# Optimization experiments

Measured on AMD Instinct MI355X. Metric: run time of the kernel, lower is better.

The kernel has to match this reference:

```python
import math
import jax, jax.numpy as jnp
import numpy as np

B, T, DIN, D, L, H = 512, 16, 7, 512, 2, 8
FF = 4 * D
HD = D // H
NEG = -1e30


def setup_inputs() -> dict:
    key = jax.random.key(0)
    ks = jax.random.split(key, 18)
    s = 0.02
    n = lambda k, sh: jax.random.normal(k, sh, dtype=jnp.float32) * s
    return {
        "x_scalar_norm": jax.random.normal(ks[0], (B, T, DIN), dtype=jnp.float32),
        "ip_w": n(ks[1], (DIN, D)),   # input_proj (x @ W)
        "ip_b": n(ks[2], (D,)),
        "qkv_w": n(ks[3], (L, D, 3 * D)),  # packed in_proj per layer
        "qkv_b": n(ks[4], (L, 3 * D)),
        "out_w": n(ks[5], (L, D, D)),
        "out_b": n(ks[6], (L, D)),
        "ln1_s": jnp.ones((L, D), jnp.float32),
        "ln1_b": jnp.zeros((L, D), jnp.float32),
        "ff_w1": n(ks[7], (L, D, FF)),
        "ff_b1": n(ks[8], (L, FF)),
        "ff_w2": n(ks[9], (L, FF, D)),
        "ff_b2": n(ks[10], (L, D)),
        "ln2_s": jnp.ones((L, D), jnp.float32),
        "ln2_b": jnp.zeros((L, D), jnp.float32),
        "head_w": n(ks[11], (D, 3)),  # moment_head
        "head_b": n(ks[12], (3,)),
    }


def _pos_encoding(t, d):
    pos = jnp.arange(t, dtype=jnp.float32)[:, None]
    div = jnp.exp(jnp.arange(0, d, 2, dtype=jnp.float32) * (-math.log(10000.0) / d))
    pe = jnp.zeros((t, d), jnp.float32)
    pe = pe.at[:, 0::2].set(jnp.sin(pos * div))
    pe = pe.at[:, 1::2].set(jnp.cos(pos * div))
    return pe


def _ln(x, s, b, eps=1e-5):
    m = jnp.mean(x, axis=-1, keepdims=True)
    v = jnp.mean(jnp.square(x - m), axis=-1, keepdims=True)
    return (x - m) * jax.lax.rsqrt(v + eps) * s + b


def _encoder_layer(h, qkv_w, qkv_b, out_w, out_b, ln1_s, ln1_b,
                   w1, b1, w2, b2, ln2_s, ln2_b, causal):
    b, t, _ = h.shape
    qkv = h @ qkv_w + qkv_b  # [b, t, 3D]
    q, k, v = jnp.split(qkv, 3, axis=-1)
    q = q.reshape(b, t, H, HD).transpose(0, 2, 1, 3)  # bhqd
    k = k.reshape(b, t, H, HD).transpose(0, 2, 1, 3)
    v = v.reshape(b, t, H, HD).transpose(0, 2, 1, 3)
    scores = jnp.einsum('bhqd,bhkd->bhqk', q, k) / math.sqrt(HD)
    scores = jnp.where(causal[None, None], scores, NEG)
    attn = jax.nn.softmax(scores, axis=-1)
    o = jnp.einsum('bhqk,bhkd->bhqd', attn, v)
    o = o.transpose(0, 2, 1, 3).reshape(b, t, D) @ out_w + out_b
    h = _ln(h + o, ln1_s, ln1_b)           # post-norm (norm_first=False)
    ff = jax.nn.relu(h @ w1 + b1) @ w2 + b2
    return _ln(h + ff, ln2_s, ln2_b)


def reference(x_scalar_norm, ip_w, ip_b, qkv_w, qkv_b, out_w, out_b,
              ln1_s, ln1_b, ff_w1, ff_b1, ff_w2, ff_b2, ln2_s, ln2_b,
              head_w, head_b):
    b, t_total, _ = x_scalar_norm.shape
    pe = _pos_encoding(t_total, D)
    x_roll = x_scalar_norm
    preds = []
    for t in range(t_total):
        xp = x_roll[:, :t + 1, :]                 # full backbone recompute per step
        h = xp @ ip_w + ip_b + pe[None, :t + 1]
        causal = jnp.tril(jnp.ones((t + 1, t + 1), dtype=bool))
        for l in range(L):
            h = _encoder_layer(h, qkv_w[l], qkv_b[l], out_w[l], out_b[l],
                               ln1_s[l], ln1_b[l], ff_w1[l], ff_b1[l],
                               ff_w2[l], ff_b2[l], ln2_s[l], ln2_b[l], causal)
        y_t = h[:, -1, :] @ head_w + head_b       # [b, 3]
        preds.append(y_t)
        if t < t_total - 1:
            # eval mode: no teacher forcing; feed back detached prediction
            x_roll = x_roll.at[:, t + 1, DIN - 3:].set(jax.lax.stop_gradient(y_t))
    return jnp.stack(preds, axis=1)  # [b, T, 3]
```

## Files before the change

### kernel.cpp

```cpp
#include <hip/hip_runtime.h>
#include <hip/hip_bf16.h>
#include <math.h>


typedef __attribute__((__ext_vector_type__(8))) short short8;
typedef __attribute__((__ext_vector_type__(4))) float floatx4;

__device__ inline short8 as_short8(uint4 v){ union U{uint4 u; short8 s;} x; x.u=v; return x.s; }

__device__ inline ushort f2bf(float f){
    __hip_bfloat16 h = __float2bfloat16(f);
    ushort u; __builtin_memcpy(&u, &h, 2); return u;
}

__device__ inline uint32_t sld32(const void* p){
    return __hip_atomic_load((const uint32_t*)p, __ATOMIC_RELAXED, __HIP_MEMORY_SCOPE_SYSTEM);
}
__device__ inline void sst32(void* p, uint32_t v){
    __hip_atomic_store((uint32_t*)p, v, __ATOMIC_RELAXED, __HIP_MEMORY_SCOPE_SYSTEM);
}
__device__ inline unsigned long long sld64(const void* p){
    return __hip_atomic_load((const unsigned long long*)p, __ATOMIC_RELAXED, __HIP_MEMORY_SCOPE_SYSTEM);
}
__device__ inline float u2f(uint32_t u){ float f; __builtin_memcpy(&f, &u, 4); return f; }

#define WS_TMPA0 12582912
#define WS_TMPA1 13631488
#define WS_TMPB0 14680064
#define WS_TMPB1 15728640
#define WS_BAR   16777216
#define WS_KC    16779264
#define WS_VC    33556480

__global__ __launch_bounds__(256)
void swz_k(const float* __restrict__ qkv_w, const float* __restrict__ out_w,
           const float* __restrict__ ff1_w, const float* __restrict__ ff2_w,
           ushort* __restrict__ wsw)
{
    if (blockIdx.z == 0){
        float* tz = (float*)((char*)wsw + WS_TMPA0);
        int id = (blockIdx.y*gridDim.x + blockIdx.x)*256 + threadIdx.x;
        sst32(&tz[id], 0u);
        sst32(&tz[id + 524288], 0u);
        if (blockIdx.x == 0 && blockIdx.y == 0){
            unsigned* bar = (unsigned*)((char*)wsw + WS_BAR);
            for (int i = threadIdx.x; i < 512; i += 256)
                sst32(&bar[i], 0u);
        }
    }
    int id = blockIdx.z; int l = id & 1; int mi = id >> 1;
    int K, N; const float* src; size_t doff;
    if (mi == 0)      { K = 512;  N = 1536; src = qkv_w + (size_t)l*786432;  doff = (size_t)l*786432; }
    else if (mi == 1) { K = 512;  N = 512;  src = out_w + (size_t)l*262144;  doff = 1572864 + (size_t)l*262144; }
    else if (mi == 2) { K = 512;  N = 2048; src = ff1_w + (size_t)l*1048576; doff = 2097152 + (size_t)l*1048576; }
    else              { K = 2048; N = 512;  src = ff2_w + (size_t)l*1048576; doff = 4194304 + (size_t)l*1048576; }
    int n0 = blockIdx.x * 64, k0 = blockIdx.y * 32;
    if (n0 >= N || k0 >= K) return;
    __shared__ float tt[32][64];
    int tid = threadIdx.x;
    int c = tid & 63, r = tid >> 6;
    #pragma unroll
    for (int i = 0; i < 8; ++i)
        tt[r + i*4][c] = src[(size_t)(k0 + r + i*4)*N + n0 + c];
    __syncthreads();
    int q = tid >> 6, n = tid & 63;
    union { ushort s[8]; uint4 v; } pk;
    #pragma unroll
    for (int i = 0; i < 8; ++i) pk.s[i] = f2bf(tt[q*8 + i][n]);
    ((uint4*)(wsw + doff))[(size_t)((k0 >> 5)*4 + q)*N + n0 + n] = pk.v;
}

#define AOX(c, m) ((((c) << 4)) + (((m) ^ ((c) & 15))))

__global__ __launch_bounds__(1024, 1)
void mega_k(const float* __restrict__ x, const float* __restrict__ ip_w,
            const float* __restrict__ ip_b, const float* __restrict__ qkv_b,
            const float* __restrict__ out_b, const float* __restrict__ ln1_s,
            const float* __restrict__ ln1_b, const float* __restrict__ ff_b1,
            const float* __restrict__ ff_b2, const float* __restrict__ ln2_s,
            const float* __restrict__ ln2_b, const float* __restrict__ hw,
            const float* __restrict__ hb, float* __restrict__ out,
            char* __restrict__ ws)
{
    const ushort* wsw = (const ushort*)ws;
    unsigned* bar = (unsigned*)(ws + WS_BAR);
    __hip_bfloat16* kc0 = (__hip_bfloat16*)(ws + WS_KC);
    __hip_bfloat16* vc0 = (__hip_bfloat16*)(ws + WS_VC);

    const int g  = blockIdx.x & 31;
    const int j  = blockIdx.x >> 5;
    const int b0 = g * 16;
    const int tid  = threadIdx.x;
    const int lane = tid & 63, w = tid >> 6;
    const int qd = lane >> 4, ln = lane & 15;
    unsigned* cnt = bar + g*16;
    unsigned epoch = 0;

    __shared__ uint4 aLds[64*16];
    __shared__ uint4 aoLds[8*16];
    __shared__ uint4 ffLds[32*16];
    __shared__ float hL[16][516];
    __shared__ float qLds[16][68];
    __shared__ float yLds[16][3];

    auto gbar = [&]() {
        __syncthreads();
        epoch += 8;
        if (tid == 0){
            __hip_atomic_fetch_add(cnt, 1u, __ATOMIC_RELAXED, __HIP_MEMORY_SCOPE_SYSTEM);
            while (__hip_atomic_load(cnt, __ATOMIC_RELAXED, __HIP_MEMORY_SCOPE_SYSTEM) < epoch)
                __builtin_amdgcn_s_sleep(8);
        }
        __syncthreads();
    };

    for (int s = 0; s < 32; ++s){
        const int t = s >> 1, l = s & 1, p = s & 1;
        __hip_bfloat16* kc = kc0 + (size_t)l*4194304;
        __hip_bfloat16* vc = vc0 + (size_t)l*4194304;
        float* tmpA = (float*)(ws + WS_TMPA0 + (size_t)p*1048576);

        if (s == 0){
            int m = tid >> 6, cg = tid & 63;
            int b = b0 + m;
            const float* xr = x + ((size_t)b*16 + 0)*7;
            float hv[8]; union { ushort sx[8]; uint4 v; } pk;
            #pragma unroll
            for (int k = 0; k < 8; ++k){
                int d = cg*8 + k;
                float pe = (d & 1) ? 1.0f : 0.0f;
                float acc = ip_b[d] + pe
                    + xr[0]*ip_w[d]        + xr[1]*ip_w[512 + d]
                    + xr[2]*ip_w[1024 + d] + xr[3]*ip_w[1536 + d]
                    + xr[4]*ip_w[2048 + d] + xr[5]*ip_w[2560 + d] + xr[6]*ip_w[3072 + d];
                hv[k] = acc; pk.sx[k] = f2bf(acc);
                hL[m][d] = acc;
            }
            aLds[AOX(cg, m)] = pk.v;
        } else {
            const float* tB = (const float*)(ws + WS_TMPB0 + (size_t)((s-1)&1)*1048576);
            const int lp = (s-1) & 1;
            int m = w, b = b0 + m;
            const float* rowp = tB + (size_t)b*512 + lane*8;
            union { unsigned long long q[4]; float f[8]; } uu;
            uu.q[0] = sld64(rowp);     uu.q[1] = sld64(rowp + 2);
            uu.q[2] = sld64(rowp + 4); uu.q[3] = sld64(rowp + 6);
            float sm = 0.f, sq = 0.f;
            #pragma unroll
            for (int k = 0; k < 8; ++k){ sm += uu.f[k]; sq += uu.f[k]*uu.f[k]; }
            #pragma unroll
            for (int off = 32; off; off >>= 1){ sm += __shfl_xor(sm, off); sq += __shfl_xor(sq, off); }
            float mean = sm * (1.0f/512.0f);
            float var  = sq * (1.0f/512.0f) - mean*mean;
            float rs   = rsqrtf(var + 1e-5f);
            float hn[8];
            #pragma unroll
            for (int k = 0; k < 8; ++k){
                int d = lane*8 + k;
                hn[k] = (uu.f[k] - mean)*rs*ln2_s[lp*512 + d] + ln2_b[lp*512 + d];
            }
            if (l == 1){
                union { ushort sx[8]; uint4 v; } pk;
                #pragma unroll
                for (int k = 0; k < 8; ++k){ hL[m][lane*8 + k] = hn[k]; pk.sx[k] = f2bf(hn[k]); }
                aLds[AOX(lane, m)] = pk.v;
            } else {
                float sr[3] = {};
                #pragma unroll
                for (int k = 0; k < 8; ++k){
                    int d = lane*8 + k;
                    sr[0] += hn[k]*hw[d*3+0]; sr[1] += hn[k]*hw[d*3+1]; sr[2] += hn[k]*hw[d*3+2];
                }
                #pragma unroll
                for (int off = 32; off; off >>= 1){
                    sr[0] += __shfl_xor(sr[0], off);
                    sr[1] += __shfl_xor(sr[1], off);
                    sr[2] += __shfl_xor(sr[2], off);
                }
                if (lane == 0){
                    #pragma unroll
                    for (int c = 0; c < 3; ++c){
                        float y = sr[c] + hb[c];
                        yLds[m][c] = y;
                        if (j == 0) out[((size_t)b*16 + (t-1))*3 + c] = y;
                    }
                }
                __syncthreads();
                int m2 = tid >> 6, cg = tid & 63;
                int b2 = b0 + m2;
                const float* xr = x + ((size_t)b2*16 + t)*7;
                float f4 = yLds[m2][0], f5 = yLds[m2][1], f6 = yLds[m2][2];
                float hv[8]; union { ushort sx[8]; uint4 v; } pk;
                #pragma unroll
                for (int k = 0; k < 8; ++k){
                    int d = cg*8 + k;
                    int e2 = d & ~1;
                    float div = expf(-(float)e2 * (9.210340371976184f / 512.0f));
                    float arg = (float)t * div;
                    float pe = (d & 1) ? cosf(arg) : sinf(arg);
                    float acc = ip_b[d] + pe
                        + xr[0]*ip_w[d]        + xr[1]*ip_w[512 + d]
                        + xr[2]*ip_w[1024 + d] + xr[3]*ip_w[1536 + d]
                        + f4*ip_w[2048 + d]    + f5*ip_w[2560 + d] + f6*ip_w[3072 + d];
                    hv[k] = acc; pk.sx[k] = f2bf(acc);
                    hL[m2][d] = acc;
                }
                aLds[AOX(cg, m2)] = pk.v;
            }
        }
        __syncthreads();

        {
            if (w < 12){
                const uint4* Bg = (const uint4*)(wsw + (size_t)l*786432);
                int s0 = w >> 2, cs = w & 3;
                floatx4 acc = {};
                for (int kb = 0; kb < 16; ++kb){
                    short8 af = as_short8(aLds[AOX(kb*4 + qd, ln)]);
                    int n = s0*512 + j*64 + cs*16 + ln;
                    short8 bf = as_short8(Bg[(size_t)(kb*4 + qd)*1536 + n]);
                    acc = __builtin_amdgcn_mfma_f32_16x16x32_bf16(af, bf, acc, 0, 0, 0);
                }
                #pragma unroll
                for (int r = 0; r < 4; ++r){
                    int row = qd*4 + r;
                    int cc = cs*16 + ln;
                    int n = s0*512 + j*64 + cc;
                    float v = acc[r] + qkv_b[l*1536 + n];
                    int b = b0 + row;
                    if (s0 == 0) qLds[row][cc] = v;
                    else if (s0 == 1) kc[(((size_t)b*8 + j)*16 + t)*64 + cc] = __float2bfloat16(v);
                    else              vc[(((size_t)b*8 + j)*16 + t)*64 + cc] = __float2bfloat16(v);
                }
            }
        }
        __syncthreads();

        {
            int m = w, b = b0 + m;
            float q = qLds[m][lane];
            const __hip_bfloat16* kp = kc + ((size_t)b*8 + j)*1024;
            const __hip_bfloat16* vp = vc + ((size_t)b*8 + j)*1024;
            float mr = -1e30f, sden = 0.0f, o = 0.0f;
            for (int jj = 0; jj <= t; ++jj){
                float pdot = q * __bfloat162float(kp[jj*64 + lane]);
                #pragma unroll
                for (int off = 32; off; off >>= 1) pdot += __shfl_xor(pdot, off);
                pdot *= 0.125f;
                float nm = fmaxf(mr, pdot);
                float sc = __expf(mr - nm);
                float e  = __expf(pdot - nm);
                sden = sden*sc + e;
                o = o*sc + e*__bfloat162float(vp[jj*64 + lane]);
                mr = nm;
            }
            float ov = o / sden;
            ((ushort*)aoLds)[AOX(lane >> 3, m)*8 + (lane & 7)] = f2bf(ov);
        }
        __syncthreads();

        {
            const uint4* Bg = (const uint4*)(wsw + 1572864 + (size_t)l*262144);
            #pragma unroll
            for (int c2 = 0; c2 < 2; ++c2){
                int n = (w*2 + c2)*16 + ln;
                floatx4 acc = {};
                #pragma unroll
                for (int kbl = 0; kbl < 2; ++kbl){
                    short8 af = as_short8(aoLds[AOX(kbl*4 + qd, ln)]);
                    short8 bf = as_short8(Bg[(size_t)((2*j + kbl)*4 + qd)*512 + n]);
                    acc = __builtin_amdgcn_mfma_f32_16x16x32_bf16(af, bf, acc, 0, 0, 0);
                }
                #pragma unroll
                for (int r = 0; r < 4; ++r){
                    int row = qd*4 + r, b = b0 + row;
                    float v = acc[r];
                    if (j == 0) v += out_b[l*512 + n] + hL[row][n];
                    unsafeAtomicAdd(&tmpA[(size_t)b*512 + n], v);
                }
            }
        }
        gbar();

        {
            float* zA = (float*)(ws + WS_TMPA0 + (size_t)((s+1)&1)*1048576);
            float* zB = (float*)(ws + WS_TMPB0 + (size_t)((s+1)&1)*1048576);
            int zr = b0 + (tid >> 6), zc = j*64 + (tid & 63);
            sst32(&zA[(size_t)zr*512 + zc], 0u);
            sst32(&zB[(size_t)zr*512 + zc], 0u);

            int m = w, b = b0 + m;
            const float* rowp = tmpA + (size_t)b*512 + lane*8;
            union { unsigned long long q[4]; float f[8]; } uu;
            uu.q[0] = sld64(rowp);     uu.q[1] = sld64(rowp + 2);
            uu.q[2] = sld64(rowp + 4); uu.q[3] = sld64(rowp + 6);
            float sm = 0.f, sq = 0.f;
            #pragma unroll
            for (int k = 0; k < 8; ++k){ sm += uu.f[k]; sq += uu.f[k]*uu.f[k]; }
            #pragma unroll
            for (int off = 32; off; off >>= 1){ sm += __shfl_xor(sm, off); sq += __shfl_xor(sq, off); }
            float mean = sm * (1.0f/512.0f);
            float var  = sq * (1.0f/512.0f) - mean*mean;
            float rs   = rsqrtf(var + 1e-5f);
            union { ushort sx[8]; uint4 v; } pk;
            #pragma unroll
            for (int k = 0; k < 8; ++k){
                int d = lane*8 + k;
                float nv = (uu.f[k] - mean)*rs*ln1_s[l*512 + d] + ln1_b[l*512 + d];
                hL[m][d] = nv;
                pk.sx[k] = f2bf(nv);
            }
            aLds[AOX(lane, m)] = pk.v;
        }
        __syncthreads();

        {
            const uint4* Bg = (const uint4*)(wsw + 2097152 + (size_t)l*1048576);
            floatx4 acc = {};
            int n = j*256 + w*16 + ln;
            for (int kb = 0; kb < 16; ++kb){
                short8 af = as_short8(aLds[AOX(kb*4 + qd, ln)]);
                short8 bf = as_short8(Bg[(size_t)(kb*4 + qd)*2048 + n]);
                acc = __builtin_amdgcn_mfma_f32_16x16x32_bf16(af, bf, acc, 0, 0, 0);
            }
            int kloc = w*16 + ln;
            #pragma unroll
            for (int r = 0; r < 4; ++r){
                int row = qd*4 + r;
                float vr = fmaxf(acc[r] + ff_b1[l*2048 + n], 0.0f);
                ((ushort*)ffLds)[AOX(kloc >> 3, row)*8 + (kloc & 7)] = f2bf(vr);
            }
        }
        __syncthreads();

        {
            const uint4* Bg = (const uint4*)(wsw + 4194304 + (size_t)l*1048576);
            float* tmpB = (float*)(ws + WS_TMPB0 + (size_t)p*1048576);
            #pragma unroll
            for (int c2 = 0; c2 < 2; ++c2){
                int n = (w*2 + c2)*16 + ln;
                floatx4 acc = {};
                #pragma unroll
                for (int kbl = 0; kbl < 8; ++kbl){
                    short8 af = as_short8(ffLds[AOX(kbl*4 + qd, ln)]);
                    short8 bf = as_short8(Bg[(size_t)((8*j + kbl)*4 + qd)*512 + n]);
                    acc = __builtin_amdgcn_mfma_f32_16x16x32_bf16(af, bf, acc, 0, 0, 0);
                }
                #pragma unroll
                for (int r = 0; r < 4; ++r){
                    int row = qd*4 + r, b = b0 + row;
                    float v = acc[r];
                    if (j == 0) v += ff_b2[l*512 + n] + hL[row][n];
                    unsafeAtomicAdd(&tmpB[(size_t)b*512 + n], v);
                }
            }
        }
        gbar();
    }

    if (j == 0){
        const float* tB = (const float*)(ws + WS_TMPB0 + (size_t)1*1048576);
        int m = w, b = b0 + m;
        const float* rowp = tB + (size_t)b*512 + lane*8;
        union { unsigned long long q[4]; float f[8]; } uu;
        uu.q[0] = sld64(rowp);     uu.q[1] = sld64(rowp + 2);
        uu.q[2] = sld64(rowp + 4); uu.q[3] = sld64(rowp + 6);
        float sm = 0.f, sq = 0.f;
        #pragma unroll
        for (int k = 0; k < 8; ++k){ sm += uu.f[k]; sq += uu.f[k]*uu.f[k]; }
        #pragma unroll
        for (int off = 32; off; off >>= 1){ sm += __shfl_xor(sm, off); sq += __shfl_xor(sq, off); }
        float mean = sm * (1.0f/512.0f);
        float var  = sq * (1.0f/512.0f) - mean*mean;
        float rs   = rsqrtf(var + 1e-5f);
        float sr[3] = {};
        #pragma unroll
        for (int k = 0; k < 8; ++k){
            int d = lane*8 + k;
            float hn = (uu.f[k] - mean)*rs*ln2_s[512 + d] + ln2_b[512 + d];
            sr[0] += hn*hw[d*3+0]; sr[1] += hn*hw[d*3+1]; sr[2] += hn*hw[d*3+2];
        }
        #pragma unroll
        for (int off = 32; off; off >>= 1){
            sr[0] += __shfl_xor(sr[0], off);
            sr[1] += __shfl_xor(sr[1], off);
            sr[2] += __shfl_xor(sr[2], off);
        }
        if (lane == 0){
            #pragma unroll
            for (int c = 0; c < 3; ++c)
                out[((size_t)b*16 + 15)*3 + c] = sr[c] + hb[c];
        }
    }
}

extern "C" void kernel_launch(void* const* d_in, const int* in_sizes, int n_in,
                              void* d_out, int out_size, void* d_ws, size_t ws_size,
                              hipStream_t stream)
{
    const float* x     = (const float*)d_in[0];
    const float* ip_w  = (const float*)d_in[1];
    const float* ip_b  = (const float*)d_in[2];
    const float* qkv_w = (const float*)d_in[3];
    const float* qkv_b = (const float*)d_in[4];
    const float* out_w = (const float*)d_in[5];
    const float* out_b = (const float*)d_in[6];
    const float* ln1_s = (const float*)d_in[7];
    const float* ln1_b = (const float*)d_in[8];
    const float* ff_w1 = (const float*)d_in[9];
    const float* ff_b1 = (const float*)d_in[10];
    const float* ff_w2 = (const float*)d_in[11];
    const float* ff_b2 = (const float*)d_in[12];
    const float* ln2_s = (const float*)d_in[13];
    const float* ln2_b = (const float*)d_in[14];
    const float* hw    = (const float*)d_in[15];
    const float* hb    = (const float*)d_in[16];
    float* outp = (float*)d_out;
    char* wsc   = (char*)d_ws;

    swz_k<<<dim3(32, 64, 8), 256, 0, stream>>>(qkv_w, out_w, ff_w1, ff_w2, (ushort*)d_ws);

    mega_k<<<dim3(256), dim3(1024), 0, stream>>>(
        x, ip_w, ip_b, qkv_b, out_b, ln1_s, ln1_b,
        ff_b1, ff_b2, ln2_s, ln2_b, hw, hb, outp, wsc);
}
```

Measured before the change: 2.455 ms.

## Pipeline weight loads through LDS with async global_load_lds in GEMM stages

Weight B-fragment loads in the QKV, FF1 and FF2 MFMA loops now go through a per-wave 4-deep LDS staging ring filled by global_load_lds. Manual vmcnt waits keep up to four loads in flight while MFMAs consume earlier stages. The goal is to hide global-memory latency that the simple per-iteration dependent load exposed. The grid barrier spin sleep is also shortened, and the change adds LDS usage plus inline-asm waitcnt fragility.

```diff
diff --git a/kernel.cpp b/kernel.cpp
--- a/kernel.cpp
+++ b/kernel.cpp
@@ -23,6 +23,12 @@
     return __hip_atomic_load((const unsigned long long*)p, __ATOMIC_RELAXED, __HIP_MEMORY_SCOPE_SYSTEM);
 }
 __device__ inline float u2f(uint32_t u){ float f; __builtin_memcpy(&f, &u, 4); return f; }
+
+__device__ inline void gld16(const void* g, void* l){
+    __builtin_amdgcn_global_load_lds(
+        (const __attribute__((address_space(1))) uint32_t*)(g),
+        (__attribute__((address_space(3))) uint32_t*)(l), 16, 0, 0);
+}
 
 #define WS_TMPA0 12582912
 #define WS_TMPA1 13631488
@@ -72,6 +78,24 @@
 
 #define AOX(c, m) ((((c) << 4)) + (((m) ^ ((c) & 15))))
 
+#define PSTEP(f, Ns, CONSUME) { \
+    asm volatile("s_waitcnt vmcnt(" Ns ")" ::: "memory"); \
+    __builtin_amdgcn_sched_barrier(0); \
+    short8 _bf = as_short8(stg[w][(f)&3][lane]); \
+    CONSUME(f, _bf); \
+    asm volatile("s_waitcnt lgkmcnt(0)" ::: "memory"); }
+
+#define PIPE16(ISSUE, CONSUME) \
+    ISSUE(0); ISSUE(1); ISSUE(2); ISSUE(3); \
+    PSTEP(0,"3",CONSUME)  ISSUE(4);  PSTEP(1,"3",CONSUME)  ISSUE(5); \
+    PSTEP(2,"3",CONSUME)  ISSUE(6);  PSTEP(3,"3",CONSUME)  ISSUE(7); \
+    PSTEP(4,"3",CONSUME)  ISSUE(8);  PSTEP(5,"3",CONSUME)  ISSUE(9); \
+    PSTEP(6,"3",CONSUME)  ISSUE(10); PSTEP(7,"3",CONSUME)  ISSUE(11); \
+    PSTEP(8,"3",CONSUME)  ISSUE(12); PSTEP(9,"3",CONSUME)  ISSUE(13); \
+    PSTEP(10,"3",CONSUME) ISSUE(14); PSTEP(11,"3",CONSUME) ISSUE(15); \
+    PSTEP(12,"3",CONSUME) PSTEP(13,"2",CONSUME) \
+    PSTEP(14,"1",CONSUME) PSTEP(15,"0",CONSUME)
+
 __global__ __launch_bounds__(1024, 1)
 void mega_k(const float* __restrict__ x, const float* __restrict__ ip_w,
             const float* __restrict__ ip_b, const float* __restrict__ qkv_b,
@@ -96,6 +120,7 @@
     unsigned* cnt = bar + g*16;
     unsigned epoch = 0;
 
+    __shared__ uint4 stg[16][4][64];
     __shared__ uint4 aLds[64*16];
     __shared__ uint4 aoLds[8*16];
     __shared__ uint4 ffLds[32*16];
@@ -109,7 +134,7 @@
         if (tid == 0){
             __hip_atomic_fetch_add(cnt, 1u, __ATOMIC_RELAXED, __HIP_MEMORY_SCOPE_SYSTEM);
             while (__hip_atomic_load(cnt, __ATOMIC_RELAXED, __HIP_MEMORY_SCOPE_SYSTEM) < epoch)
-                __builtin_amdgcn_s_sleep(8);
+                __builtin_amdgcn_s_sleep(2);
         }
         __syncthreads();
     };
@@ -214,13 +239,14 @@
             if (w < 12){
                 const uint4* Bg = (const uint4*)(wsw + (size_t)l*786432);
                 int s0 = w >> 2, cs = w & 3;
+                const int nidx = s0*512 + j*64 + cs*16 + ln;
                 floatx4 acc = {};
-                for (int kb = 0; kb < 16; ++kb){
-                    short8 af = as_short8(aLds[AOX(kb*4 + qd, ln)]);
-                    int n = s0*512 + j*64 + cs*16 + ln;
-                    short8 bf = as_short8(Bg[(size_t)(kb*4 + qd)*1536 + n]);
-                    acc = __builtin_amdgcn_mfma_f32_16x16x32_bf16(af, bf, acc, 0, 0, 0);
-                }
+#define QISS(f) gld16(&Bg[(size_t)((f)*4 + qd)*1536 + nidx], &stg[w][(f)&3][0])
+#define QCON(f, bfr) acc = __builtin_amdgcn_mfma_f32_16x16x32_bf16( \
+                    as_short8(aLds[AOX((f)*4 + qd, ln)]), bfr, acc, 0, 0, 0)
+                PIPE16(QISS, QCON)
+#undef QISS
+#undef QCON
                 #pragma unroll
                 for (int r = 0; r < 4; ++r){
                     int row = qd*4 + r;
@@ -316,18 +342,19 @@
 
         {
             const uint4* Bg = (const uint4*)(wsw + 2097152 + (size_t)l*1048576);
+            const int n1 = j*256 + w*16 + ln;
             floatx4 acc = {};
-            int n = j*256 + w*16 + ln;
-            for (int kb = 0; kb < 16; ++kb){
-                short8 af = as_short8(aLds[AOX(kb*4 + qd, ln)]);
-                short8 bf = as_short8(Bg[(size_t)(kb*4 + qd)*2048 + n]);
-                acc = __builtin_amdgcn_mfma_f32_16x16x32_bf16(af, bf, acc, 0, 0, 0);
-            }
+#define F1ISS(f) gld16(&Bg[(size_t)((f)*4 + qd)*2048 + n1], &stg[w][(f)&3][0])
+#define F1CON(f, bfr) acc = __builtin_amdgcn_mfma_f32_16x16x32_bf16( \
+                as_short8(aLds[AOX((f)*4 + qd, ln)]), bfr, acc, 0, 0, 0)
+            PIPE16(F1ISS, F1CON)
+#undef F1ISS
+#undef F1CON
             int kloc = w*16 + ln;
             #pragma unroll
             for (int r = 0; r < 4; ++r){
                 int row = qd*4 + r;
-                float vr = fmaxf(acc[r] + ff_b1[l*2048 + n], 0.0f);
+                float vr = fmaxf(acc[r] + ff_b1[l*2048 + n1], 0.0f);
                 ((ushort*)ffLds)[AOX(kloc >> 3, row)*8 + (kloc & 7)] = f2bf(vr);
             }
         }
@@ -336,20 +363,21 @@
         {
             const uint4* Bg = (const uint4*)(wsw + 4194304 + (size_t)l*1048576);
             float* tmpB = (float*)(ws + WS_TMPB0 + (size_t)p*1048576);
+            floatx4 acc2[2] = {};
+#define F2ISS(f) gld16(&Bg[(size_t)((8*j + ((f)&7))*4 + qd)*512 + (w*2 + ((f)>>3))*16 + ln], \
+                       &stg[w][(f)&3][0])
+#define F2CON(f, bfr) acc2[(f)>>3] = __builtin_amdgcn_mfma_f32_16x16x32_bf16( \
+                as_short8(ffLds[AOX(((f)&7)*4 + qd, ln)]), bfr, acc2[(f)>>3], 0, 0, 0)
+            PIPE16(F2ISS, F2CON)
+#undef F2ISS
+#undef F2CON
             #pragma unroll
             for (int c2 = 0; c2 < 2; ++c2){
                 int n = (w*2 + c2)*16 + ln;
-                floatx4 acc = {};
-                #pragma unroll
-                for (int kbl = 0; kbl < 8; ++kbl){
-                    short8 af = as_short8(ffLds[AOX(kbl*4 + qd, ln)]);
-                    short8 bf = as_short8(Bg[(size_t)((8*j + kbl)*4 + qd)*512 + n]);
-                    acc = __builtin_amdgcn_mfma_f32_16x16x32_bf16(af, bf, acc, 0, 0, 0);
-                }
                 #pragma unroll
                 for (int r = 0; r < 4; ++r){
                     int row = qd*4 + r, b = b0 + row;
-                    float v = acc[r];
+                    float v = acc2[c2][r];
                     if (j == 0) v += ff_b2[l*512 + n] + hL[row][n];
                     unsafeAtomicAdd(&tmpB[(size_t)b*512 + n], v);
                 }
```

New measurement: 2.289 ms. 1.07x faster.
